# Kernel optimization log

Hardware: AMD Instinct MI355X
Metric: run time of the kernel (lower is better)

## Reference

```python
import jax, jax.numpy as jnp
import numpy as np

B = 32768
P = 32  # max_poles == max_zeros
NC = P + 1  # count classes 0..32
BIG = 1e30

POLE_COUNT_W = 5.0
ZERO_COUNT_W = 5.0
POLE_VALUE_W = 1.0
ZERO_VALUE_W = 1.0


def setup_inputs() -> dict:
    key = jax.random.key(0)
    ks = jax.random.split(key, 8)
    return {
        "pole_count_logits": jax.random.normal(ks[0], (B, NC), jnp.float32),
        "zero_count_logits": jax.random.normal(ks[1], (B, NC), jnp.float32),
        "poles_all": jax.random.normal(ks[2], (B, P, 2), jnp.float32),
        "zeros_all": jax.random.normal(ks[3], (B, P, 2), jnp.float32),
        "target_poles_pad": jax.random.normal(ks[4], (B, P, 2), jnp.float32),
        "target_zeros_pad": jax.random.normal(ks[5], (B, P, 2), jnp.float32),
        "target_num_poles": jax.random.randint(ks[6], (B,), 0, NC, jnp.int32),
        "target_num_zeros": jax.random.randint(ks[7], (B,), 0, NC, jnp.int32),
    }


def _cross_entropy(logits, targets):
    logp = jax.nn.log_softmax(logits, axis=-1)
    nll = -jnp.take_along_axis(logp, targets[:, None].astype(jnp.int32), axis=1)[:, 0]
    return jnp.mean(nll)


def _masked_chamfer(pred, tgt, n_pred, n_tgt):
    """Vectorized variable-length chamfer. pred/tgt: [B,P,2], counts: [B]."""
    ar = jnp.arange(pred.shape[1])
    pm = ar[None, :] < n_pred[:, None]  # [B,P] valid pred mask
    tm = ar[None, :] < n_tgt[:, None]   # [B,P] valid target mask
    diff = pred[:, :, None, :] - tgt[:, None, :, :]  # [B,P,T,2]
    d = jnp.sum(diff * diff, axis=-1)                # [B,P,T] |z_p - z_t|^2
    min_p2t = jnp.min(jnp.where(tm[:, None, :], d, BIG), axis=2)  # [B,P]
    mean_p2t = jnp.sum(jnp.where(pm, min_p2t, 0.0), axis=1) / jnp.maximum(n_pred, 1).astype(pred.dtype)
    min_t2p = jnp.min(jnp.where(pm[:, :, None], d, BIG), axis=1)  # [B,T]
    mean_t2p = jnp.sum(jnp.where(tm, min_t2p, 0.0), axis=1) / jnp.maximum(n_tgt, 1).astype(pred.dtype)
    both = mean_p2t + mean_t2p
    sum_tgt_sq = jnp.sum(jnp.where(tm[:, :, None], tgt * tgt, 0.0), axis=(1, 2))
    sum_pred_sq = jnp.sum(jnp.where(pm[:, :, None], pred * pred, 0.0), axis=(1, 2))
    p0 = n_pred == 0
    t0 = n_tgt == 0
    out = jnp.where(p0 & t0, 0.0,
          jnp.where(p0, sum_tgt_sq,
          jnp.where(t0, sum_pred_sq, both)))
    return out  # [B]


def reference(pole_count_logits, zero_count_logits, poles_all, zeros_all,
              target_poles_pad, target_zeros_pad, target_num_poles, target_num_zeros):
    loss_pole_count = _cross_entropy(pole_count_logits, target_num_poles)
    loss_zero_count = _cross_entropy(zero_count_logits, target_num_zeros)

    pred_pole_counts = jnp.argmax(pole_count_logits, axis=-1).astype(jnp.int32)
    pred_zero_counts = jnp.argmax(zero_count_logits, axis=-1).astype(jnp.int32)

    pole_losses = _masked_chamfer(poles_all, target_poles_pad, pred_pole_counts, target_num_poles)
    zero_losses = _masked_chamfer(zeros_all, target_zeros_pad, pred_zero_counts, target_num_zeros)
    loss_pole_value = jnp.mean(pole_losses)
    loss_zero_value = jnp.mean(zero_losses)

    total_loss = (POLE_COUNT_W * loss_pole_count + ZERO_COUNT_W * loss_zero_count
                  + POLE_VALUE_W * loss_pole_value + ZERO_VALUE_W * loss_zero_value)
    return total_loss
```

## Files before the change

kernel.cpp:

```cpp
#include <hip/hip_runtime.h>
#include <float.h>

#define NCNT 33
#define NPTS 32

typedef float f32x2 __attribute__((ext_vector_type(2)));

__device__ __forceinline__ f32x2 mk2(float a, float b) { f32x2 r; r.x = a; r.y = b; return r; }

template<int CTRL, bool BC>
__device__ __forceinline__ int dpp_i(int old, int v) {
    return __builtin_amdgcn_update_dpp(old, v, CTRL, 0xF, 0xF, BC);
}

__device__ __forceinline__ float wave_sum63(float v) {
    v += __int_as_float(dpp_i<0x111, true>(0, __float_as_int(v)));
    v += __int_as_float(dpp_i<0x112, true>(0, __float_as_int(v)));
    v += __int_as_float(dpp_i<0x114, true>(0, __float_as_int(v)));
    v += __int_as_float(dpp_i<0x118, true>(0, __float_as_int(v)));
    v += __int_as_float(dpp_i<0x142, true>(0, __float_as_int(v)));
    v += __int_as_float(dpp_i<0x143, true>(0, __float_as_int(v)));
    return __int_as_float(__builtin_amdgcn_readlane(__float_as_int(v), 63));
}

__device__ __forceinline__ float wave_max63(float v) {
#define MX_STEP(C)                                                                    \
    {                                                                                 \
        int o = dpp_i<C, false>(__float_as_int(v), __float_as_int(v));                \
        v = fmaxf(v, __int_as_float(o));                                              \
    }
    MX_STEP(0x111) MX_STEP(0x112) MX_STEP(0x114) MX_STEP(0x118) MX_STEP(0x142) MX_STEP(0x143)
#undef MX_STEP
    return __int_as_float(__builtin_amdgcn_readlane(__float_as_int(v), 63));
}

__global__ __launch_bounds__(256) void vltf_kernel(
    const float* __restrict__ pole_logits, const float* __restrict__ zero_logits,
    const float* __restrict__ poles_all,   const float* __restrict__ zeros_all,
    const float* __restrict__ tpoles,      const float* __restrict__ tzeros,
    const int* __restrict__ tnum_p,        const int* __restrict__ tnum_z,
    float* __restrict__ partials)
{
    __shared__ __align__(16) float lds[4 * 192];

    const int lane = threadIdx.x & 63;
    const int wid  = threadIdx.x >> 6;
    const int unit = (blockIdx.x << 2) | wid;
    const int row  = unit >> 1;
    const int part = unit & 1;
    float* myl = lds + wid * 192;

    const float* logits = part ? zero_logits : pole_logits;
    const float* predp  = part ? zeros_all   : poles_all;
    const float* tgtp   = part ? tzeros      : tpoles;
    const int*   tnum   = part ? tnum_z      : tnum_p;

    float x = (lane < NCNT) ? logits[row * NCNT + lane] : -FLT_MAX;
    float vmax = wave_max63(x);
    unsigned long long bm = __ballot(lane < NCNT && x == vmax);
    const int np = (int)__builtin_ctzll(bm);
    float e = (lane < NCNT) ? __expf(x - vmax) : 0.f;
    float sume = wave_sum63(e);
    const int nt = tnum[row];
    float xt = __int_as_float(__builtin_amdgcn_readlane(__float_as_int(x), nt));
    float nll = vmax + __logf(sume) - xt;

    const bool isPred = lane < 32;
    const int  idx    = lane & 31;
    const float2* ownArr = (const float2*)(isPred ? predp : tgtp);
    const float2  Pt     = ownArr[row * NPTS + idx];
    const int  nown = isPred ? np : nt;
    const bool vown = idx < nown;
    const float sreal = fmaf(Pt.x, Pt.x, Pt.y * Pt.y);

    const int wbase = isPred ? 96 : 0;
    const int uvpos = wbase + ((idx >> 1) << 2) + (idx & 1);
    myl[uvpos]            = vown ? -2.f * Pt.x : 0.f;
    myl[uvpos + 2]        = vown ? -2.f * Pt.y : 0.f;
    myl[wbase + 64 + idx] = vown ? sreal : 1e30f;
    __syncthreads();

    const int rbase = isPred ? 0 : 96;
    const float4* UVo = (const float4*)(myl + rbase);
    const float4* So  = (const float4*)(myl + rbase + 64);
    const f32x2 Pxv = mk2(Pt.x, Pt.x);
    const f32x2 Pyv = mk2(Pt.y, Pt.y);
    float m = FLT_MAX;
#pragma unroll
    for (int i = 0; i < 8; ++i) {
        float4 uv0 = UVo[2 * i], uv1 = UVo[2 * i + 1];
        float4 s4  = So[i];
        f32x2 val0 = Pyv * mk2(uv0.z, uv0.w) + mk2(s4.x, s4.y);
        val0       = Pxv * mk2(uv0.x, uv0.y) + val0;
        f32x2 val1 = Pyv * mk2(uv1.z, uv1.w) + mk2(s4.z, s4.w);
        val1       = Pxv * mk2(uv1.x, uv1.y) + val1;
        m = fminf(m, fminf(val0.x, val0.y));
        m = fminf(m, fminf(val1.x, val1.y));
    }

    float T;
    if (np > 0 && nt > 0) {
        float inv_n = __builtin_amdgcn_rcpf((float)nown);
        T = vown ? (m + sreal) * inv_n : 0.f;
    } else if (np == 0 && nt == 0) {
        T = 0.f;
    } else if (np == 0) {
        T = (!isPred && vown) ? sreal : 0.f;
    } else {
        T = (isPred && vown) ? sreal : 0.f;
    }
    float cham = wave_sum63(T);

    if (lane == 0) partials[unit] = 5.f * nll + cham;
}

__global__ __launch_bounds__(1024) void vltf_finalize(
    const float4* __restrict__ p4, int n4, float invB, float* __restrict__ out)
{
    float s = 0.f;
    for (int i = threadIdx.x; i < n4; i += 1024) {
        float4 v = p4[i];
        s += (v.x + v.y) + (v.z + v.w);
    }
    s = wave_sum63(s);
    __shared__ float sh[16];
    if ((threadIdx.x & 63) == 0) sh[threadIdx.x >> 6] = s;
    __syncthreads();
    if (threadIdx.x == 0) {
        float t = 0.f;
#pragma unroll
        for (int i = 0; i < 16; ++i) t += sh[i];
        out[0] = t * invB;
    }
}

extern "C" void kernel_launch(void* const* d_in, const int* in_sizes, int n_in,
                              void* d_out, int out_size, void* d_ws, size_t ws_size,
                              hipStream_t stream) {
    const float* pole_logits = (const float*)d_in[0];
    const float* zero_logits = (const float*)d_in[1];
    const float* poles_all   = (const float*)d_in[2];
    const float* zeros_all   = (const float*)d_in[3];
    const float* tpoles      = (const float*)d_in[4];
    const float* tzeros      = (const float*)d_in[5];
    const int*   tnp         = (const int*)d_in[6];
    const int*   tnz         = (const int*)d_in[7];

    const int B     = in_sizes[6];
    const int units = 2 * B;

    float* partials = (float*)d_ws;

    vltf_kernel<<<units / 4, 256, 0, stream>>>(pole_logits, zero_logits,
                                               poles_all, zeros_all,
                                               tpoles, tzeros, tnp, tnz, partials);
    vltf_finalize<<<1, 1024, 0, stream>>>((const float4*)partials, units / 4,
                                          1.0f / (float)B, (float*)d_out);
}
```

Before: 112.0 us.

## Convert per-row waves into a persistent grid-stride loop with next-row prefetch

```diff
diff --git a/kernel.cpp b/kernel.cpp
--- a/kernel.cpp
+++ b/kernel.cpp
@@ -39,79 +39,96 @@
     const float* __restrict__ poles_all,   const float* __restrict__ zeros_all,
     const float* __restrict__ tpoles,      const float* __restrict__ tzeros,
     const int* __restrict__ tnum_p,        const int* __restrict__ tnum_z,
-    float* __restrict__ partials)
+    float* __restrict__ partials, int B)
 {
     __shared__ __align__(16) float lds[4 * 192];
 
     const int lane = threadIdx.x & 63;
     const int wid  = threadIdx.x >> 6;
-    const int unit = (blockIdx.x << 2) | wid;
-    const int row  = unit >> 1;
-    const int part = unit & 1;
+    const int w    = (blockIdx.x << 2) | wid;
+    const int W    = gridDim.x << 2;
     float* myl = lds + wid * 192;
 
-    const float* logits = part ? zero_logits : pole_logits;
-    const float* predp  = part ? zeros_all   : poles_all;
-    const float* tgtp   = part ? tzeros      : tpoles;
-    const int*   tnum   = part ? tnum_z      : tnum_p;
-
-    float x = (lane < NCNT) ? logits[row * NCNT + lane] : -FLT_MAX;
-    float vmax = wave_max63(x);
-    unsigned long long bm = __ballot(lane < NCNT && x == vmax);
-    const int np = (int)__builtin_ctzll(bm);
-    float e = (lane < NCNT) ? __expf(x - vmax) : 0.f;
-    float sume = wave_sum63(e);
-    const int nt = tnum[row];
-    float xt = __int_as_float(__builtin_amdgcn_readlane(__float_as_int(x), nt));
-    float nll = vmax + __logf(sume) - xt;
-
+    const int  part   = w & 1;
     const bool isPred = lane < 32;
     const int  idx    = lane & 31;
-    const float2* ownArr = (const float2*)(isPred ? predp : tgtp);
-    const float2  Pt     = ownArr[row * NPTS + idx];
-    const int  nown = isPred ? np : nt;
-    const bool vown = idx < nown;
-    const float sreal = fmaf(Pt.x, Pt.x, Pt.y * Pt.y);
 
-    const int wbase = isPred ? 96 : 0;
-    const int uvpos = wbase + ((idx >> 1) << 2) + (idx & 1);
-    myl[uvpos]            = vown ? -2.f * Pt.x : 0.f;
-    myl[uvpos + 2]        = vown ? -2.f * Pt.y : 0.f;
-    myl[wbase + 64 + idx] = vown ? sreal : 1e30f;
-    __syncthreads();
+    const float* logits  = part ? zero_logits : pole_logits;
+    const float2* ownArr = (const float2*)(part ? (isPred ? zeros_all : tzeros)
+                                                : (isPred ? poles_all : tpoles));
+    const int* tnum      = part ? tnum_z : tnum_p;
 
-    const int rbase = isPred ? 0 : 96;
-    const float4* UVo = (const float4*)(myl + rbase);
-    const float4* So  = (const float4*)(myl + rbase + 64);
-    const f32x2 Pxv = mk2(Pt.x, Pt.x);
-    const f32x2 Pyv = mk2(Pt.y, Pt.y);
-    float m = FLT_MAX;
+    const int r0      = w >> 1;
+    const int rstride = W >> 1;
+    if (r0 >= B) return;
+
+    float  x_n  = (lane < NCNT) ? logits[r0 * NCNT + lane] : -FLT_MAX;
+    float2 Pt_n = ownArr[r0 * NPTS + idx];
+    int    nt_n = tnum[r0];
+
+    for (int r = r0; r < B; r += rstride) {
+        const float  x  = x_n;
+        const float2 Pt = Pt_n;
+        const int    nt = nt_n;
+
+        const int rn = r + rstride;
+        if (rn < B) {
+            x_n  = (lane < NCNT) ? logits[rn * NCNT + lane] : -FLT_MAX;
+            Pt_n = ownArr[rn * NPTS + idx];
+            nt_n = tnum[rn];
+        }
+
+        float vmax = wave_max63(x);
+        unsigned long long bm = __ballot(lane < NCNT && x == vmax);
+        const int np = (int)__builtin_ctzll(bm);
+        float e = (lane < NCNT) ? __expf(x - vmax) : 0.f;
+        float sume = wave_sum63(e);
+        float xt = __int_as_float(__builtin_amdgcn_readlane(__float_as_int(x), nt));
+        float nll = vmax + __logf(sume) - xt;
+
+        const int  nown  = isPred ? np : nt;
+        const bool vown  = idx < nown;
+        const float sreal = fmaf(Pt.x, Pt.x, Pt.y * Pt.y);
+
+        const int wbase = isPred ? 96 : 0;
+        const int uvpos = wbase + ((idx >> 1) << 2) + (idx & 1);
+        myl[uvpos]            = vown ? -2.f * Pt.x : 0.f;
+        myl[uvpos + 2]        = vown ? -2.f * Pt.y : 0.f;
+        myl[wbase + 64 + idx] = vown ? sreal : 1e30f;
+
+        const int rbase = isPred ? 0 : 96;
+        const float4* UVo = (const float4*)(myl + rbase);
+        const float4* So  = (const float4*)(myl + rbase + 64);
+        const f32x2 Pxv = mk2(Pt.x, Pt.x);
+        const f32x2 Pyv = mk2(Pt.y, Pt.y);
+        float m = FLT_MAX;
 #pragma unroll
-    for (int i = 0; i < 8; ++i) {
-        float4 uv0 = UVo[2 * i], uv1 = UVo[2 * i + 1];
-        float4 s4  = So[i];
-        f32x2 val0 = Pyv * mk2(uv0.z, uv0.w) + mk2(s4.x, s4.y);
-        val0       = Pxv * mk2(uv0.x, uv0.y) + val0;
-        f32x2 val1 = Pyv * mk2(uv1.z, uv1.w) + mk2(s4.z, s4.w);
-        val1       = Pxv * mk2(uv1.x, uv1.y) + val1;
-        m = fminf(m, fminf(val0.x, val0.y));
-        m = fminf(m, fminf(val1.x, val1.y));
+        for (int i = 0; i < 8; ++i) {
+            float4 uv0 = UVo[2 * i], uv1 = UVo[2 * i + 1];
+            float4 s4  = So[i];
+            f32x2 val0 = Pyv * mk2(uv0.z, uv0.w) + mk2(s4.x, s4.y);
+            val0       = Pxv * mk2(uv0.x, uv0.y) + val0;
+            f32x2 val1 = Pyv * mk2(uv1.z, uv1.w) + mk2(s4.z, s4.w);
+            val1       = Pxv * mk2(uv1.x, uv1.y) + val1;
+            m = fminf(m, fminf(val0.x, val0.y));
+            m = fminf(m, fminf(val1.x, val1.y));
+        }
+
+        float T;
+        if (np > 0 && nt > 0) {
+            float inv_n = __builtin_amdgcn_rcpf((float)nown);
+            T = vown ? (m + sreal) * inv_n : 0.f;
+        } else if (np == 0 && nt == 0) {
+            T = 0.f;
+        } else if (np == 0) {
+            T = (!isPred && vown) ? sreal : 0.f;
+        } else {
+            T = (isPred && vown) ? sreal : 0.f;
+        }
+        float cham = wave_sum63(T);
+
+        if (lane == 0) partials[2 * r + part] = 5.f * nll + cham;
     }
-
-    float T;
-    if (np > 0 && nt > 0) {
-        float inv_n = __builtin_amdgcn_rcpf((float)nown);
-        T = vown ? (m + sreal) * inv_n : 0.f;
-    } else if (np == 0 && nt == 0) {
-        T = 0.f;
-    } else if (np == 0) {
-        T = (!isPred && vown) ? sreal : 0.f;
-    } else {
-        T = (isPred && vown) ? sreal : 0.f;
-    }
-    float cham = wave_sum63(T);
-
-    if (lane == 0) partials[unit] = 5.f * nll + cham;
 }
 
 __global__ __launch_bounds__(1024) void vltf_finalize(
@@ -151,9 +168,11 @@
 
     float* partials = (float*)d_ws;
 
-    vltf_kernel<<<units / 4, 256, 0, stream>>>(pole_logits, zero_logits,
-                                               poles_all, zeros_all,
-                                               tpoles, tzeros, tnp, tnz, partials);
+    int blocks = 2048;
+    if (blocks * 4 > units) blocks = (units + 3) / 4;
+    vltf_kernel<<<blocks, 256, 0, stream>>>(pole_logits, zero_logits,
+                                            poles_all, zeros_all,
+                                            tpoles, tzeros, tnp, tnz, partials, B);
     vltf_finalize<<<1, 1024, 0, stream>>>((const float4*)partials, units / 4,
                                           1.0f / (float)B, (float*)d_out);
 }
```

Result: no change. 113.1 us (+1.0%).
